# Kernel optimization log

Measured on AMD Instinct MI355X. Metric: run time of the kernel, lower is better.

Reference implementation:

```python
import jax, jax.numpy as jnp
import numpy as np

S = 64.0  # scale
M = 0.35  # margin


def setup_inputs() -> dict:
    key = jax.random.key(0)
    k1, k2 = jax.random.split(key)
    B, C = 1024, 100000
    x = jax.random.uniform(k1, (B, C), dtype=jnp.float32)  # cosine-like logits in [0,1)
    label = jax.random.randint(k2, (B,), 0, C, dtype=jnp.int64)
    return {"x": x, "label": label}


def reference(x, label):
    B = x.shape[0]
    rows = jnp.arange(B)
    x_y = x[rows, label]                      # [B] target logit per sample
    numerator = S * (x_y - M)                 # margin-adjusted, scaled
    exp_sx = jnp.exp(S * x)                   # [B, C] single elementwise pass
    # sum over j != label  ==  full row sum minus the target term
    sum_excl = jnp.sum(exp_sx, axis=1) - jnp.exp(S * x_y)
    denominator = jnp.exp(numerator) + sum_excl
    L = (numerator - jnp.log(denominator)) / S
    return -jnp.mean(L)
```

## Files before the change

### kernel.cpp

```cpp
#include <hip/hip_runtime.h>
#include <math.h>


#define SCALE 64.0f
#define MARGIN 0.35f
#define NT 512

__device__ __forceinline__ double block_reduce_d(double v) {
    #pragma unroll
    for (int off = 32; off > 0; off >>= 1) v += __shfl_down(v, off, 64);
    __shared__ double s[NT / 64];
    const int lane = threadIdx.x & 63;
    const int w    = threadIdx.x >> 6;
    if (lane == 0) s[w] = v;
    __syncthreads();
    if (w == 0) {
        v = (lane < NT / 64) ? s[lane] : 0.0;
        #pragma unroll
        for (int off = NT / 128; off > 0; off >>= 1) v += __shfl_down(v, off, 64);
    }
    return v;
}

__global__ __launch_bounds__(NT) void row_loss_kernel(
    const float* __restrict__ x, const int* __restrict__ label,
    double* __restrict__ row_L, int C)
{
    const int row = blockIdx.x;
    const float* __restrict__ xr = x + (size_t)row * (size_t)C;
    const int tid = threadIdx.x;

    const int n4 = C >> 2;
    const float4* __restrict__ x4 = (const float4*)xr;

    double acc = 0.0;
    int v = tid;
    for (; v + 3 * NT < n4; v += 4 * NT) {
        float4 a = x4[v];
        float4 b = x4[v + NT];
        float4 c = x4[v + 2 * NT];
        float4 d = x4[v + 3 * NT];
        float s0 = __expf(SCALE * a.x) + __expf(SCALE * a.y) +
                   __expf(SCALE * a.z) + __expf(SCALE * a.w);
        float s1 = __expf(SCALE * b.x) + __expf(SCALE * b.y) +
                   __expf(SCALE * b.z) + __expf(SCALE * b.w);
        float s2 = __expf(SCALE * c.x) + __expf(SCALE * c.y) +
                   __expf(SCALE * c.z) + __expf(SCALE * c.w);
        float s3 = __expf(SCALE * d.x) + __expf(SCALE * d.y) +
                   __expf(SCALE * d.z) + __expf(SCALE * d.w);
        acc += (double)(s0 + s1) + (double)(s2 + s3);
    }
    for (; v < n4; v += NT) {
        float4 a = x4[v];
        float s0 = __expf(SCALE * a.x) + __expf(SCALE * a.y) +
                   __expf(SCALE * a.z) + __expf(SCALE * a.w);
        acc += (double)s0;
    }
    for (int j = (n4 << 2) + tid; j < C; j += NT)
        acc += (double)__expf(SCALE * xr[j]);

    double row_sum = block_reduce_d(acc);

    if (tid == 0) {
        const double xy  = (double)xr[label[row]];
        const double num = 64.0 * (xy - 0.35);
        const double exy = exp(64.0 * xy);
        const double sum_excl = row_sum - exy;
        const double denom = exp(num) + sum_excl;
        const double L = (num - log(denom)) / 64.0;
        row_L[row] = L;
    }
}

__global__ __launch_bounds__(NT) void final_reduce_kernel(
    const double* __restrict__ row_L, float* __restrict__ out, int B)
{
    double acc = 0.0;
    for (int i = threadIdx.x; i < B; i += NT) acc += row_L[i];
    double total = block_reduce_d(acc);
    if (threadIdx.x == 0) out[0] = (float)(-total / (double)B);
}

extern "C" void kernel_launch(void* const* d_in, const int* in_sizes, int n_in,
                              void* d_out, int out_size, void* d_ws, size_t ws_size,
                              hipStream_t stream) {
    const float* x     = (const float*)d_in[0];
    const int*   label = (const int*)d_in[1];
    const int B = in_sizes[1];
    const int C = in_sizes[0] / B;

    double* row_L = (double*)d_ws;

    row_loss_kernel<<<B, NT, 0, stream>>>(x, label, row_L, C);
    final_reduce_kernel<<<1, NT, 0, stream>>>(row_L, (float*)d_out, B);
}
```

Before: 512.4 us.

## Split each row across multiple blocks and move per-row loss to finalize kernel

Each row is now reduced by several smaller blocks that write partial sums, instead of one 512-thread block per row. The per-row loss computation moves into a single 1024-thread finalize kernel that also performs the mean. Loads switch to nontemporal vector loads to avoid polluting the caches with streaming data. The split is meant to raise the number of blocks and improve memory-level parallelism, at the cost of a small partials buffer and a serial finalize step.

Result: faster. 499.4 us (-2.5%).

```diff
diff --git a/kernel.cpp b/kernel.cpp
--- a/kernel.cpp
+++ b/kernel.cpp
@@ -4,42 +4,48 @@
 
 #define SCALE 64.0f
 #define MARGIN 0.35f
-#define NT 512
+#define NT 256
+#define GSPLIT 4
 
+typedef float v4f __attribute__((ext_vector_type(4)));
+
+template <int NWAVES>
 __device__ __forceinline__ double block_reduce_d(double v) {
     #pragma unroll
     for (int off = 32; off > 0; off >>= 1) v += __shfl_down(v, off, 64);
-    __shared__ double s[NT / 64];
+    __shared__ double s[NWAVES];
     const int lane = threadIdx.x & 63;
     const int w    = threadIdx.x >> 6;
     if (lane == 0) s[w] = v;
     __syncthreads();
     if (w == 0) {
-        v = (lane < NT / 64) ? s[lane] : 0.0;
+        v = (lane < NWAVES) ? s[lane] : 0.0;
         #pragma unroll
-        for (int off = NT / 128; off > 0; off >>= 1) v += __shfl_down(v, off, 64);
+        for (int off = NWAVES / 2; off > 0; off >>= 1) v += __shfl_down(v, off, 64);
     }
     return v;
 }
 
-__global__ __launch_bounds__(NT) void row_loss_kernel(
-    const float* __restrict__ x, const int* __restrict__ label,
-    double* __restrict__ row_L, int C)
+__global__ __launch_bounds__(NT) void partial_sum_kernel(
+    const float* __restrict__ x, double* __restrict__ partials, int C)
 {
-    const int row = blockIdx.x;
+    const int g   = blockIdx.x;
+    const int row = blockIdx.y;
     const float* __restrict__ xr = x + (size_t)row * (size_t)C;
     const int tid = threadIdx.x;
 
-    const int n4 = C >> 2;
-    const float4* __restrict__ x4 = (const float4*)xr;
+    const int n4    = C >> 2;
+    const int begin = (int)(((long long)n4 * g) / GSPLIT);
+    const int end   = (int)(((long long)n4 * (g + 1)) / GSPLIT);
+    const v4f* __restrict__ x4 = (const v4f*)xr;
 
     double acc = 0.0;
-    int v = tid;
-    for (; v + 3 * NT < n4; v += 4 * NT) {
-        float4 a = x4[v];
-        float4 b = x4[v + NT];
-        float4 c = x4[v + 2 * NT];
-        float4 d = x4[v + 3 * NT];
+    int v = begin + tid;
+    for (; v + 3 * NT < end; v += 4 * NT) {
+        v4f a = __builtin_nontemporal_load(x4 + v);
+        v4f b = __builtin_nontemporal_load(x4 + v + NT);
+        v4f c = __builtin_nontemporal_load(x4 + v + 2 * NT);
+        v4f d = __builtin_nontemporal_load(x4 + v + 3 * NT);
         float s0 = __expf(SCALE * a.x) + __expf(SCALE * a.y) +
                    __expf(SCALE * a.z) + __expf(SCALE * a.w);
         float s1 = __expf(SCALE * b.x) + __expf(SCALE * b.y) +
@@ -50,34 +56,37 @@
                    __expf(SCALE * d.z) + __expf(SCALE * d.w);
         acc += (double)(s0 + s1) + (double)(s2 + s3);
     }
-    for (; v < n4; v += NT) {
-        float4 a = x4[v];
-        float s0 = __expf(SCALE * a.x) + __expf(SCALE * a.y) +
-                   __expf(SCALE * a.z) + __expf(SCALE * a.w);
-        acc += (double)s0;
+    for (; v < end; v += NT) {
+        v4f a = __builtin_nontemporal_load(x4 + v);
+        acc += (double)(__expf(SCALE * a.x) + __expf(SCALE * a.y) +
+                        __expf(SCALE * a.z) + __expf(SCALE * a.w));
     }
-    for (int j = (n4 << 2) + tid; j < C; j += NT)
-        acc += (double)__expf(SCALE * xr[j]);
+    if (g == GSPLIT - 1) {
+        for (int j = (n4 << 2) + tid; j < C; j += NT)
+            acc += (double)__expf(SCALE * xr[j]);
+    }
 
-    double row_sum = block_reduce_d(acc);
+    double s = block_reduce_d<NT / 64>(acc);
+    if (tid == 0) partials[(size_t)row * GSPLIT + g] = s;
+}
 
-    if (tid == 0) {
-        const double xy  = (double)xr[label[row]];
+__global__ __launch_bounds__(1024) void finalize_kernel(
+    const float* __restrict__ x, const int* __restrict__ label,
+    const double* __restrict__ partials, float* __restrict__ out, int B, int C)
+{
+    double acc = 0.0;
+    for (int row = threadIdx.x; row < B; row += 1024) {
+        double rs = 0.0;
+        #pragma unroll
+        for (int g = 0; g < GSPLIT; ++g) rs += partials[(size_t)row * GSPLIT + g];
+        const double xy  = (double)x[(size_t)row * (size_t)C + label[row]];
         const double num = 64.0 * (xy - 0.35);
         const double exy = exp(64.0 * xy);
-        const double sum_excl = row_sum - exy;
+        const double sum_excl = rs - exy;
         const double denom = exp(num) + sum_excl;
-        const double L = (num - log(denom)) / 64.0;
-        row_L[row] = L;
+        acc += (num - log(denom)) / 64.0;
     }
-}
-
-__global__ __launch_bounds__(NT) void final_reduce_kernel(
-    const double* __restrict__ row_L, float* __restrict__ out, int B)
-{
-    double acc = 0.0;
-    for (int i = threadIdx.x; i < B; i += NT) acc += row_L[i];
-    double total = block_reduce_d(acc);
+    double total = block_reduce_d<16>(acc);
     if (threadIdx.x == 0) out[0] = (float)(-total / (double)B);
 }
 
@@ -89,8 +98,9 @@
     const int B = in_sizes[1];
     const int C = in_sizes[0] / B;
 
-    double* row_L = (double*)d_ws;
+    double* partials = (double*)d_ws;
 
-    row_loss_kernel<<<B, NT, 0, stream>>>(x, label, row_L, C);
-    final_reduce_kernel<<<1, NT, 0, stream>>>(row_L, (float*)d_out, B);
+    dim3 grid1(GSPLIT, B);
+    partial_sum_kernel<<<grid1, NT, 0, stream>>>(x, partials, C);
+    finalize_kernel<<<1, 1024, 0, stream>>>(x, label, partials, (float*)d_out, B, C);
 }
```
